# Kernel tuning notes

Hardware: AMD Instinct MI355X
Metric: run time of the kernel (lower is better)

Reference implementation:

```python
import jax, jax.numpy as jnp
import numpy as np
from math import sqrt

B, N, DK = 4, 4096, 64


def setup_inputs() -> dict:
    key = jax.random.key(0)
    ks = jax.random.split(key, 5)
    x = jax.random.normal(ks[0], (B, N, DK), dtype=jnp.float32)
    Wv = jax.random.normal(ks[1], (DK, DK), dtype=jnp.float32) / sqrt(DK)
    bv = jax.random.normal(ks[2], (DK,), dtype=jnp.float32) * 0.02
    wq = jax.random.normal(ks[3], (DK,), dtype=jnp.float32) / sqrt(DK)
    wk = jax.random.normal(ks[4], (DK,), dtype=jnp.float32) / sqrt(DK)
    gamma = jnp.ones((DK,), dtype=jnp.float32)
    beta = jnp.zeros((DK,), dtype=jnp.float32)
    return {"x": x, "Wv": Wv, "bv": bv, "wq": wq, "wk": wk, "gamma": gamma, "beta": beta}


def _layer_norm(h, gamma, beta, eps=1e-5):
    mu = jnp.mean(h, axis=-1, keepdims=True)
    var = jnp.var(h, axis=-1, keepdims=True)
    return (h - mu) * jax.lax.rsqrt(var + eps) * gamma + beta


def reference(x, Wv, bv, wq, wk, gamma, beta):
    d_k = x.shape[-1]
    V = jnp.einsum('bnd,ed->bne', x, Wv) + bv          # (B, N, DK)
    Q = jnp.einsum('bnd,d->bn', x, wq)                 # scalar per token
    K = jnp.einsum('bnd,d->bn', x, wk)
    # RBF-kernel scores A[b,i,j] = exp(-(Q_i - K_j)^2)  -> (B, N, N)
    A = jnp.exp(-jnp.square(Q[:, :, None] - K[:, None, :]))
    P = jax.nn.softmax(A / sqrt(d_k), axis=-1)
    out = jnp.einsum('bij,bjd->bid', P, V) + x
    return _layer_norm(out, gamma, beta)
```

## Files before the change

### kernel.cpp

```cpp
#include <hip/hip_runtime.h>

#define NB   4
#define NSEQ 4096
#define DK   64
#define NTOK (NB * NSEQ)

#define QK_SCALE 1.2011224087864498f

typedef __attribute__((ext_vector_type(8))) _Float16 half8;
typedef __attribute__((ext_vector_type(2))) _Float16 half2v;
typedef __attribute__((ext_vector_type(2))) __fp16 fp16x2;
typedef __attribute__((ext_vector_type(4))) float f32x4;

__device__ __forceinline__ float fast_exp2(float x) {
#if __has_builtin(__builtin_amdgcn_exp2f)
    return __builtin_amdgcn_exp2f(x);
#else
    return exp2f(x);
#endif
}

__device__ __forceinline__ half2v pack_f16(float a, float b) {
#if __has_builtin(__builtin_amdgcn_cvt_pkrtz)
    union { fp16x2 f; half2v h; } c;
    c.f = __builtin_amdgcn_cvt_pkrtz(a, b);
    return c.h;
#else
    half2v r; r[0] = (_Float16)a; r[1] = (_Float16)b; return r;
#endif
}

__device__ __forceinline__ half8 u4_to_h8(uint4 u) {
    union { uint4 u; half8 h; } c; c.u = u; return c.h;
}

#define AS3U(p) ((__attribute__((address_space(3))) unsigned int*)(p))
#define AS1U(p) ((const __attribute__((address_space(1))) unsigned int*)(p))


__global__ __launch_bounds__(512) void qkv_kernel(
    const float* __restrict__ x, const float* __restrict__ Wv,
    const float* __restrict__ bv, const float* __restrict__ wq,
    const float* __restrict__ wk,
    float* __restrict__ Qs, float* __restrict__ Ks, unsigned short* __restrict__ Vt)
{
    __shared__ float x_lds[64 * 68];
    __shared__ float wvt[64 * 68];
    __shared__ float wqk[128];
    __shared__ float bvl[64];
    __shared__ unsigned short vt_lds[64 * 72];

    const int t = threadIdx.x;
    const int tok0 = blockIdx.x * 64;

    #pragma unroll
    for (int r = 0; r < 2; ++r) {
        int f = t + 512 * r;
        int row = f >> 4, c4 = f & 15;
        float4 v = ((const float4*)(x + (size_t)(tok0 + row) * DK))[c4];
        *(float4*)&x_lds[row * 68 + c4 * 4] = v;
    }
    #pragma unroll
    for (int r = 0; r < 2; ++r) {
        int f = t + 512 * r;
        int e = f >> 4, c4 = f & 15;
        float4 v = ((const float4*)(Wv + e * DK))[c4];
        wvt[(c4 * 4 + 0) * 68 + e] = v.x;
        wvt[(c4 * 4 + 1) * 68 + e] = v.y;
        wvt[(c4 * 4 + 2) * 68 + e] = v.z;
        wvt[(c4 * 4 + 3) * 68 + e] = v.w;
    }
    if (t < 64) { wqk[t * 2] = wq[t]; wqk[t * 2 + 1] = wk[t]; bvl[t] = bv[t]; }
    __syncthreads();

    const int tok = t >> 3, oc = t & 7;
    const int e0 = oc * 8;
    float acc[8];
    #pragma unroll
    for (int ee = 0; ee < 8; ++ee) acc[ee] = bvl[e0 + ee];

    for (int d = 0; d < DK; d += 4) {
        float4 x4 = *(const float4*)&x_lds[tok * 68 + d];
        const float xs[4] = {x4.x, x4.y, x4.z, x4.w};
        #pragma unroll
        for (int dd = 0; dd < 4; ++dd) {
            float xv = xs[dd];
            const float4* wrow = (const float4*)&wvt[(d + dd) * 68 + e0];
            float4 wa = wrow[0], wb = wrow[1];
            acc[0] += xv * wa.x; acc[1] += xv * wa.y;
            acc[2] += xv * wa.z; acc[3] += xv * wa.w;
            acc[4] += xv * wb.x; acc[5] += xv * wb.y;
            acc[6] += xv * wb.z; acc[7] += xv * wb.w;
        }
    }
    #pragma unroll
    for (int k = 0; k < 8; ++k) {
        _Float16 hv = (_Float16)acc[k];
        vt_lds[(e0 + k) * 72 + tok] = *(unsigned short*)&hv;
    }

    if (t < 128) {
        const int tk = t & 63;
        const int sel = (t >= 64);
        float a = 0.f;
        for (int d = 0; d < DK; ++d)
            a += x_lds[tk * 68 + d] * wqk[d * 2 + sel];
        (sel ? Ks : Qs)[tok0 + tk] = a * QK_SCALE;
    }
    __syncthreads();

    const int bb = tok0 >> 12, n0 = tok0 & 4095;
    {
        const int c = t >> 6, d = t & 63;
        uint4 v = *(const uint4*)((const char*)vt_lds + d * 144 + c * 16);
        const int jc   = (n0 >> 5) + (c >> 2);
        const int lane = (c & 3) * 16 + (d & 15);
        const int ct   = d >> 4;
        unsigned short* dst = Vt + ((((size_t)bb * 128 + jc) * 4 + ct) * 64 + lane) * 8;
        *(uint4*)dst = v;
    }
}

extern __shared__ float smem[];

__global__ __launch_bounds__(1024, 4) void attn_kernel(
    const float* __restrict__ x,
    const float* __restrict__ Qsg, const float* __restrict__ Ksg,
    const unsigned short* __restrict__ Vt,
    const float* __restrict__ gamma, const float* __restrict__ beta,
    float* __restrict__ out, int nrep)
{
    float* k_lds = smem;
    unsigned short* vs = (unsigned short*)(smem + 4096);
    float* red   = smem + 4096;
    float* dred  = smem + 4096 + 8 * 64 * 68;

    const int t    = threadIdx.x;
    const int B    = blockIdx.x;
    const int b    = (B & 7) >> 1;
    const int i0   = (((B >> 3) << 1) | (B & 1)) << 6;
    const int w    = t >> 6;
    const int lane = t & 63;
    const int rit  = lane & 15;
    const int q    = lane >> 4;
    const int rgrp = w >> 3;
    const int js   = w & 7;

    ((float4*)k_lds)[t] = ((const float4*)(Ksg + (size_t)b * 4096))[t];

    const float Qs0 = Qsg[b * 4096 + i0 + rgrp * 32 + rit];
    const float Qs1 = Qsg[b * 4096 + i0 + rgrp * 32 + 16 + rit];

    const _Float16 onef = (_Float16)1.0f;
    const half8 vones = {onef, onef, onef, onef, onef, onef, onef, onef};
    const half2v c2 = {(_Float16)3.2552083e-4f, (_Float16)3.2552083e-4f};
    const half2v c1 = {(_Float16)7.8125e-3f, (_Float16)7.8125e-3f};
    const half2v c0 = {(_Float16)0.125f, (_Float16)0.125f};
    const half2v h1 = {onef, onef};

    const unsigned short* Vtb0 = Vt + (size_t)b * 262144;

    for (int rep = 0; rep < nrep; ++rep) {

    f32x4 acc[2][4] = {};
    f32x4 accd[2] = {};

    #pragma unroll
    for (int i = 0; i < 4; ++i) {
        const int row = w + 16 * i;
        const unsigned short* g = Vtb0 + row * 512 + lane * 8;
        unsigned short* l = vs + row * 512;
#if __has_builtin(__builtin_amdgcn_global_load_lds)
        __builtin_amdgcn_global_load_lds(AS1U(g), AS3U(l), 16, 0, 0);
#else
        *(uint4*)(l + lane * 8) = *(const uint4*)g;
#endif
    }
    __syncthreads();

    for (int r = 0; r < 8; ++r) {
        const int bf = r & 1;
        if (r < 7) {
            #pragma unroll
            for (int i = 0; i < 4; ++i) {
                const int row = w + 16 * i;
                const unsigned short* g = Vtb0 + (r + 1) * 32768 + row * 512 + lane * 8;
                unsigned short* l = vs + (bf ^ 1) * 32768 + row * 512;
#if __has_builtin(__builtin_amdgcn_global_load_lds)
                __builtin_amdgcn_global_load_lds(AS1U(g), AS3U(l), 16, 0, 0);
#else
                *(uint4*)(l + lane * 8) = *(const uint4*)g;
#endif
            }
        }

        #pragma unroll
        for (int sl = 0; sl < 2; ++sl) {
            const int jcl = js * 2 + sl;
            const unsigned short* vf = vs + bf * 32768 + jcl * 2048 + lane * 8;
            uint4 bu0 = *(const uint4*)(vf);
            uint4 bu1 = *(const uint4*)(vf + 512);
            uint4 bu2 = *(const uint4*)(vf + 1024);
            uint4 bu3 = *(const uint4*)(vf + 1536);

            const float* kn = k_lds + r * 512 + jcl * 32 + q * 8;
            float4 ka = *(const float4*)(kn);
            float4 kb = *(const float4*)(kn + 4);
            float kv[8] = {ka.x, ka.y, ka.z, ka.w, kb.x, kb.y, kb.z, kb.w};

            half2v w0p[4], w1p[4];
            #pragma unroll
            for (int jp = 0; jp < 4; ++jp) {
                float d0a = Qs0 - kv[2 * jp],     d0b = Qs0 - kv[2 * jp + 1];
                float g0a = fast_exp2(-d0a * d0a), g0b = fast_exp2(-d0b * d0b);
                half2v g0 = pack_f16(g0a, g0b);
                w0p[jp] = g0 * (g0 * (g0 * c2 + c1) + c0) + h1;

                float d1a = Qs1 - kv[2 * jp],     d1b = Qs1 - kv[2 * jp + 1];
                float g1a = fast_exp2(-d1a * d1a), g1b = fast_exp2(-d1b * d1b);
                half2v g1 = pack_f16(g1a, g1b);
                w1p[jp] = g1 * (g1 * (g1 * c2 + c1) + c0) + h1;
            }
            union { half2v p[4]; half8 h; } ua0, ua1;
            #pragma unroll
            for (int jp = 0; jp < 4; ++jp) { ua0.p[jp] = w0p[jp]; ua1.p[jp] = w1p[jp]; }
            half8 a0 = ua0.h, a1 = ua1.h;

            half8 b0 = u4_to_h8(bu0), b1 = u4_to_h8(bu1);
            half8 b2 = u4_to_h8(bu2), b3 = u4_to_h8(bu3);
            acc[0][0] = __builtin_amdgcn_mfma_f32_16x16x32_f16(a0, b0, acc[0][0], 0, 0, 0);
            acc[0][1] = __builtin_amdgcn_mfma_f32_16x16x32_f16(a0, b1, acc[0][1], 0, 0, 0);
            acc[0][2] = __builtin_amdgcn_mfma_f32_16x16x32_f16(a0, b2, acc[0][2], 0, 0, 0);
            acc[0][3] = __builtin_amdgcn_mfma_f32_16x16x32_f16(a0, b3, acc[0][3], 0, 0, 0);
            acc[1][0] = __builtin_amdgcn_mfma_f32_16x16x32_f16(a1, b0, acc[1][0], 0, 0, 0);
            acc[1][1] = __builtin_amdgcn_mfma_f32_16x16x32_f16(a1, b1, acc[1][1], 0, 0, 0);
            acc[1][2] = __builtin_amdgcn_mfma_f32_16x16x32_f16(a1, b2, acc[1][2], 0, 0, 0);
            acc[1][3] = __builtin_amdgcn_mfma_f32_16x16x32_f16(a1, b3, acc[1][3], 0, 0, 0);
            accd[0]   = __builtin_amdgcn_mfma_f32_16x16x32_f16(a0, vones, accd[0], 0, 0, 0);
            accd[1]   = __builtin_amdgcn_mfma_f32_16x16x32_f16(a1, vones, accd[1], 0, 0, 0);
        }
        __syncthreads();
    }

    {
        float* rbase = red + (size_t)js * (64 * 68);
        #pragma unroll
        for (int rt = 0; rt < 2; ++rt)
            #pragma unroll
            for (int ct = 0; ct < 4; ++ct)
                #pragma unroll
                for (int rg = 0; rg < 4; ++rg)
                    rbase[(rgrp * 32 + rt * 16 + q * 4 + rg) * 68 + ct * 16 + rit]
                        = acc[rt][ct][rg];
        if (rit == 0) {
            #pragma unroll
            for (int rt = 0; rt < 2; ++rt)
                #pragma unroll
                for (int rg = 0; rg < 4; ++rg)
                    dred[js * 64 + rgrp * 32 + rt * 16 + q * 4 + rg] = accd[rt][rg];
        }
    }
    __syncthreads();

    {
        const int row = t >> 4, cg = t & 15, c0i = cg * 4;
        float dsum = 0.f;
        #pragma unroll
        for (int sl = 0; sl < 8; ++sl) dsum += dred[sl * 64 + row];
        const float inv = 1.0f / dsum;
        const size_t rowg = (size_t)(b * 4096 + i0 + row);

        float4 num = make_float4(0.f, 0.f, 0.f, 0.f);
        #pragma unroll
        for (int sl = 0; sl < 8; ++sl) {
            float4 r4 = *(const float4*)&red[(size_t)sl * (64 * 68) + row * 68 + c0i];
            num.x += r4.x; num.y += r4.y; num.z += r4.z; num.w += r4.w;
        }
        const float4 x4 = *(const float4*)(x + rowg * 64 + c0i);
        float4 h;
        h.x = num.x * inv + x4.x;
        h.y = num.y * inv + x4.y;
        h.z = num.z * inv + x4.z;
        h.w = num.w * inv + x4.w;

        float sm = h.x + h.y + h.z + h.w;
        float ss = h.x * h.x + h.y * h.y + h.z * h.z + h.w * h.w;
        #pragma unroll
        for (int m = 1; m < 16; m <<= 1) { sm += __shfl_xor(sm, m); ss += __shfl_xor(ss, m); }
        const float mu   = sm * 0.015625f;
        const float var  = ss * 0.015625f - mu * mu;
        const float rstd = rsqrtf(var + 1e-5f);

        const float4 g4 = *(const float4*)(gamma + c0i);
        const float4 b4 = *(const float4*)(beta + c0i);
        float4 o;
        o.x = (h.x - mu) * rstd * g4.x + b4.x;
        o.y = (h.y - mu) * rstd * g4.y + b4.y;
        o.z = (h.z - mu) * rstd * g4.z + b4.z;
        o.w = (h.w - mu) * rstd * g4.w + b4.w;
        *(float4*)(out + rowg * 64 + c0i) = o;
    }
    __syncthreads();
    }
}

extern "C" void kernel_launch(void* const* d_in, const int* in_sizes, int n_in,
                              void* d_out, int out_size, void* d_ws, size_t ws_size,
                              hipStream_t stream)
{
    const float* x     = (const float*)d_in[0];
    const float* Wv    = (const float*)d_in[1];
    const float* bv    = (const float*)d_in[2];
    const float* wq    = (const float*)d_in[3];
    const float* wk    = (const float*)d_in[4];
    const float* gamma = (const float*)d_in[5];
    const float* beta  = (const float*)d_in[6];
    float* out = (float*)d_out;

    float* Qs = (float*)d_ws;
    float* Ks = Qs + NTOK;
    unsigned short* Vt = (unsigned short*)(Ks + NTOK);

    const int attn_lds = 4096 * 4 + 8 * 64 * 68 * 4 + 8 * 64 * 4;
    (void)hipFuncSetAttribute((const void*)attn_kernel,
                              hipFuncAttributeMaxDynamicSharedMemorySize, attn_lds);

    qkv_kernel<<<dim3(NTOK / 64), dim3(512), 0, stream>>>(x, Wv, bv, wq, wk, Qs, Ks, Vt);
    attn_kernel<<<dim3(NB * (NSEQ / 64)), dim3(1024), attn_lds, stream>>>(
        x, Qs, Ks, Vt, gamma, beta, out, 1);
}
```

Baseline: 92.96 us.

## Load V fragments directly from global memory instead of staging through LDS

Removes the double-buffered global_load_lds staging of V into shared memory along with the per-round __syncthreads. Each wave now reads its own contiguous slice of the key range straight from global memory (through the cache) over 16 chunks. This drops the block-wide barriers and LDS traffic, but global load latency is now exposed in the inner loop and there is no explicit prefetch. The reduction buffer no longer aliases the V staging area.

```diff
diff --git a/kernel.cpp b/kernel.cpp
--- a/kernel.cpp
+++ b/kernel.cpp
@@ -33,9 +33,6 @@
 __device__ __forceinline__ half8 u4_to_h8(uint4 u) {
     union { uint4 u; half8 h; } c; c.u = u; return c.h;
 }
-
-#define AS3U(p) ((__attribute__((address_space(3))) unsigned int*)(p))
-#define AS1U(p) ((const __attribute__((address_space(1))) unsigned int*)(p))
 
 
 __global__ __launch_bounds__(512) void qkv_kernel(
@@ -131,7 +128,6 @@
     float* __restrict__ out, int nrep)
 {
     float* k_lds = smem;
-    unsigned short* vs = (unsigned short*)(smem + 4096);
     float* red   = smem + 4096;
     float* dred  = smem + 4096 + 8 * 64 * 68;
 
@@ -158,88 +154,58 @@
     const half2v c0 = {(_Float16)0.125f, (_Float16)0.125f};
     const half2v h1 = {onef, onef};
 
-    const unsigned short* Vtb0 = Vt + (size_t)b * 262144;
+    const unsigned short* vb = Vt + (size_t)b * 262144 + (size_t)(js * 16) * 2048 + lane * 8;
+    const float* kp = k_lds + js * 512 + q * 8;
+
+    __syncthreads();
 
     for (int rep = 0; rep < nrep; ++rep) {
 
     f32x4 acc[2][4] = {};
     f32x4 accd[2] = {};
 
-    #pragma unroll
-    for (int i = 0; i < 4; ++i) {
-        const int row = w + 16 * i;
-        const unsigned short* g = Vtb0 + row * 512 + lane * 8;
-        unsigned short* l = vs + row * 512;
-#if __has_builtin(__builtin_amdgcn_global_load_lds)
-        __builtin_amdgcn_global_load_lds(AS1U(g), AS3U(l), 16, 0, 0);
-#else
-        *(uint4*)(l + lane * 8) = *(const uint4*)g;
-#endif
-    }
-    __syncthreads();
-
-    for (int r = 0; r < 8; ++r) {
-        const int bf = r & 1;
-        if (r < 7) {
-            #pragma unroll
-            for (int i = 0; i < 4; ++i) {
-                const int row = w + 16 * i;
-                const unsigned short* g = Vtb0 + (r + 1) * 32768 + row * 512 + lane * 8;
-                unsigned short* l = vs + (bf ^ 1) * 32768 + row * 512;
-#if __has_builtin(__builtin_amdgcn_global_load_lds)
-                __builtin_amdgcn_global_load_lds(AS1U(g), AS3U(l), 16, 0, 0);
-#else
-                *(uint4*)(l + lane * 8) = *(const uint4*)g;
-#endif
-            }
-        }
-
-        #pragma unroll
-        for (int sl = 0; sl < 2; ++sl) {
-            const int jcl = js * 2 + sl;
-            const unsigned short* vf = vs + bf * 32768 + jcl * 2048 + lane * 8;
-            uint4 bu0 = *(const uint4*)(vf);
-            uint4 bu1 = *(const uint4*)(vf + 512);
-            uint4 bu2 = *(const uint4*)(vf + 1024);
-            uint4 bu3 = *(const uint4*)(vf + 1536);
-
-            const float* kn = k_lds + r * 512 + jcl * 32 + q * 8;
-            float4 ka = *(const float4*)(kn);
-            float4 kb = *(const float4*)(kn + 4);
-            float kv[8] = {ka.x, ka.y, ka.z, ka.w, kb.x, kb.y, kb.z, kb.w};
-
-            half2v w0p[4], w1p[4];
-            #pragma unroll
-            for (int jp = 0; jp < 4; ++jp) {
-                float d0a = Qs0 - kv[2 * jp],     d0b = Qs0 - kv[2 * jp + 1];
-                float g0a = fast_exp2(-d0a * d0a), g0b = fast_exp2(-d0b * d0b);
-                half2v g0 = pack_f16(g0a, g0b);
-                w0p[jp] = g0 * (g0 * (g0 * c2 + c1) + c0) + h1;
-
-                float d1a = Qs1 - kv[2 * jp],     d1b = Qs1 - kv[2 * jp + 1];
-                float g1a = fast_exp2(-d1a * d1a), g1b = fast_exp2(-d1b * d1b);
-                half2v g1 = pack_f16(g1a, g1b);
-                w1p[jp] = g1 * (g1 * (g1 * c2 + c1) + c0) + h1;
-            }
-            union { half2v p[4]; half8 h; } ua0, ua1;
-            #pragma unroll
-            for (int jp = 0; jp < 4; ++jp) { ua0.p[jp] = w0p[jp]; ua1.p[jp] = w1p[jp]; }
-            half8 a0 = ua0.h, a1 = ua1.h;
-
-            half8 b0 = u4_to_h8(bu0), b1 = u4_to_h8(bu1);
-            half8 b2 = u4_to_h8(bu2), b3 = u4_to_h8(bu3);
-            acc[0][0] = __builtin_amdgcn_mfma_f32_16x16x32_f16(a0, b0, acc[0][0], 0, 0, 0);
-            acc[0][1] = __builtin_amdgcn_mfma_f32_16x16x32_f16(a0, b1, acc[0][1], 0, 0, 0);
-            acc[0][2] = __builtin_amdgcn_mfma_f32_16x16x32_f16(a0, b2, acc[0][2], 0, 0, 0);
-            acc[0][3] = __builtin_amdgcn_mfma_f32_16x16x32_f16(a0, b3, acc[0][3], 0, 0, 0);
-            acc[1][0] = __builtin_amdgcn_mfma_f32_16x16x32_f16(a1, b0, acc[1][0], 0, 0, 0);
-            acc[1][1] = __builtin_amdgcn_mfma_f32_16x16x32_f16(a1, b1, acc[1][1], 0, 0, 0);
-            acc[1][2] = __builtin_amdgcn_mfma_f32_16x16x32_f16(a1, b2, acc[1][2], 0, 0, 0);
-            acc[1][3] = __builtin_amdgcn_mfma_f32_16x16x32_f16(a1, b3, acc[1][3], 0, 0, 0);
-            accd[0]   = __builtin_amdgcn_mfma_f32_16x16x32_f16(a0, vones, accd[0], 0, 0, 0);
-            accd[1]   = __builtin_amdgcn_mfma_f32_16x16x32_f16(a1, vones, accd[1], 0, 0, 0);
-        }
-        __syncthreads();
+    for (int c = 0; c < 16; ++c) {
+        const unsigned short* vf = vb + c * 2048;
+        uint4 bu0 = *(const uint4*)(vf);
+        uint4 bu1 = *(const uint4*)(vf + 512);
+        uint4 bu2 = *(const uint4*)(vf + 1024);
+        uint4 bu3 = *(const uint4*)(vf + 1536);
+
+        const float* kn = kp + c * 32;
+        float4 ka = *(const float4*)(kn);
+        float4 kb = *(const float4*)(kn + 4);
+        float kv[8] = {ka.x, ka.y, ka.z, ka.w, kb.x, kb.y, kb.z, kb.w};
+
+        half2v w0p[4], w1p[4];
+        #pragma unroll
+        for (int jp = 0; jp < 4; ++jp) {
+            float d0a = Qs0 - kv[2 * jp],     d0b = Qs0 - kv[2 * jp + 1];
+            float g0a = fast_exp2(-d0a * d0a), g0b = fast_exp2(-d0b * d0b);
+            half2v g0 = pack_f16(g0a, g0b);
+            w0p[jp] = g0 * (g0 * (g0 * c2 + c1) + c0) + h1;
+
+            float d1a = Qs1 - kv[2 * jp],     d1b = Qs1 - kv[2 * jp + 1];
+            float g1a = fast_exp2(-d1a * d1a), g1b = fast_exp2(-d1b * d1b);
+            half2v g1 = pack_f16(g1a, g1b);
+            w1p[jp] = g1 * (g1 * (g1 * c2 + c1) + c0) + h1;
+        }
+        union { half2v p[4]; half8 h; } ua0, ua1;
+        #pragma unroll
+        for (int jp = 0; jp < 4; ++jp) { ua0.p[jp] = w0p[jp]; ua1.p[jp] = w1p[jp]; }
+        half8 a0 = ua0.h, a1 = ua1.h;
+
+        half8 b0 = u4_to_h8(bu0), b1 = u4_to_h8(bu1);
+        half8 b2 = u4_to_h8(bu2), b3 = u4_to_h8(bu3);
+        acc[0][0] = __builtin_amdgcn_mfma_f32_16x16x32_f16(a0, b0, acc[0][0], 0, 0, 0);
+        acc[0][1] = __builtin_amdgcn_mfma_f32_16x16x32_f16(a0, b1, acc[0][1], 0, 0, 0);
+        acc[0][2] = __builtin_amdgcn_mfma_f32_16x16x32_f16(a0, b2, acc[0][2], 0, 0, 0);
+        acc[0][3] = __builtin_amdgcn_mfma_f32_16x16x32_f16(a0, b3, acc[0][3], 0, 0, 0);
+        acc[1][0] = __builtin_amdgcn_mfma_f32_16x16x32_f16(a1, b0, acc[1][0], 0, 0, 0);
+        acc[1][1] = __builtin_amdgcn_mfma_f32_16x16x32_f16(a1, b1, acc[1][1], 0, 0, 0);
+        acc[1][2] = __builtin_amdgcn_mfma_f32_16x16x32_f16(a1, b2, acc[1][2], 0, 0, 0);
+        acc[1][3] = __builtin_amdgcn_mfma_f32_16x16x32_f16(a1, b3, acc[1][3], 0, 0, 0);
+        accd[0]   = __builtin_amdgcn_mfma_f32_16x16x32_f16(a0, vones, accd[0], 0, 0, 0);
+        accd[1]   = __builtin_amdgcn_mfma_f32_16x16x32_f16(a1, vones, accd[1], 0, 0, 0);
     }
 
     {
```

Measured after the change: 91.34 us. No clear change (-1.8%).
